# Performance work log

Measured on AMD Instinct MI355X. Metric: run time of the kernel, lower is better.

## Reference

```python
import jax, jax.numpy as jnp
import numpy as np

TOL_CONTACT = 0.01  # contact tolerance from signed_dis


def _knn_pair(ref_pts, ref_nrm, q_pts, k):
    """Signed distance from each query point to the surface of one other object.

    ref_pts/ref_nrm: [Nr,3] reference object points (in plane frame) and normals.
    q_pts: [Nq,3] query object points (in plane frame). Returns [Nq].
    """
    # brute-force squared distances [Nq, Nr] (same math as tra.nearest_neighbor)
    sq = (jnp.sum(q_pts * q_pts, -1)[:, None]
          - 2.0 * (q_pts @ ref_pts.T)
          + jnp.sum(ref_pts * ref_pts, -1)[None, :])
    negd, idx = jax.lax.top_k(-sq, k)                  # k nearest per query: [Nq,k]
    dist = jnp.sqrt(jnp.maximum(-negd, 0.0))           # euclidean distances
    near = ref_pts[idx]                                # [Nq,k,3] gathered surface pts
    near_n = ref_nrm[idx]                              # [Nq,k,3] gathered normals
    grad = near - q_pts[:, None, :]
    grad = grad / jnp.linalg.norm(grad, axis=-1, keepdims=True)
    insides = jnp.sum(near_n * grad, axis=-1) > 0      # einsum('okij,okij->oki')
    inside = jnp.sum(insides, axis=-1) > k * 0.8       # majority vote over k
    # nearest-neighbor distance, sign-flipped when inside
    return jnp.where(inside, -dist[:, 0], dist[:, 0])


def reference(points, est_T, plane_T, k):
    M, N, _ = points.shape
    # transform object points into plane frame
    T = jnp.linalg.inv(plane_T)[None] @ est_T          # [M,4,4]
    xyz = points[..., :3]
    nrm = points[..., 3:6]
    pts_pl = jnp.einsum('mij,mnj->mni', T[:, :3, :3], xyz) + T[:, None, :3, 3]
    sd_plane = pts_pl[..., 2]                          # plane signed distance [M,N]

    # signed distance of object b's points to every other object o: pair[b,o,:]
    pair = jax.vmap(
        lambda q: jax.vmap(lambda rp, rn: _knn_pair(rp, rn, q, k))(pts_pl, nrm)
    )(pts_pl)                                          # [M,M,N]
    big = jnp.asarray(jnp.finfo(pair.dtype).max, pair.dtype)
    pair = jnp.where(jnp.eye(M, dtype=bool)[:, :, None], big, pair)
    sd_obj = jnp.min(pair, axis=1)                     # min over other objects [M,N]

    signed_distance = jnp.minimum(sd_plane, sd_obj)
    intersects = signed_distance < -TOL_CONTACT
    return signed_distance, intersects


def setup_inputs() -> dict:
    key = jax.random.key(0)
    kp, kn, kt, kpl = jax.random.split(key, 4)
    M, N = 4, 3072
    # objects offset from each other so pairwise nearest distances are > 0
    xyz = jax.random.normal(kp, (M, N, 3), jnp.float32) * 0.05 \
        + jnp.arange(M, dtype=jnp.float32)[:, None, None] * 0.3
    nrm = jax.random.normal(kn, (M, N, 3), jnp.float32)
    nrm = nrm / jnp.linalg.norm(nrm, axis=-1, keepdims=True)
    points = jnp.concatenate([xyz, nrm], axis=-1)      # [M,N,6]

    def rigid(k_, n):
        q, _ = jnp.linalg.qr(jax.random.normal(k_, (n, 3, 3), jnp.float32))
        t = jax.random.normal(jax.random.fold_in(k_, 7), (n, 3), jnp.float32) * 0.1
        T = jnp.zeros((n, 4, 4), jnp.float32)
        T = T.at[:, :3, :3].set(q).at[:, :3, 3].set(t).at[:, 3, 3].set(1.0)
        return T

    est_T = rigid(kt, M)        # per-object estimated transforms [M,4,4]
    plane_T = rigid(kpl, 1)[0]  # plane transform [4,4]
    return {"points": points, "est_T": est_T, "plane_T": plane_T, "k": 10}
```

## Files before the change

kernel.cpp:

```cpp
#include <hip/hip_runtime.h>
#include <math.h>

#define M_OBJ 4
#define N_PTS 3072
#define K_NN  10
#define NSLOT (M_OBJ - 1)
#define QPB   64
#define SEG   4
#define SEGN  (N_PTS / SEG)
#define MSTR  10

__device__ inline void make_T(const float* __restrict__ E,
                              const float* __restrict__ P,
                              float T[3][4]) {
    float Pi[3][4];
#pragma unroll
    for (int i = 0; i < 3; ++i) {
#pragma unroll
        for (int j = 0; j < 3; ++j) Pi[i][j] = P[j * 4 + i];
        Pi[i][3] = -(P[0 * 4 + i] * P[3] + P[1 * 4 + i] * P[7] + P[2 * 4 + i] * P[11]);
    }
#pragma unroll
    for (int i = 0; i < 3; ++i) {
#pragma unroll
        for (int j = 0; j < 4; ++j) {
            float acc = (j == 3) ? Pi[i][3] : 0.0f;
#pragma unroll
            for (int kk = 0; kk < 3; ++kk) acc += Pi[i][kk] * E[kk * 4 + j];
            T[i][j] = acc;
        }
    }
}

__device__ __forceinline__ void insert10(float s, int id, float bs[K_NN], int bi[K_NN]) {
    bs[0] = s; bi[0] = id;
#pragma unroll
    for (int t = 0; t < K_NN - 1; ++t) {
        if (bs[t] > bs[t + 1]) {
            float a = bs[t]; bs[t] = bs[t + 1]; bs[t + 1] = a;
            int   b = bi[t]; bi[t] = bi[t + 1]; bi[t + 1] = b;
        }
    }
}

__device__ __forceinline__ float score(const float4 p, float qx, float qy, float qz) {
    return fmaf(p.x, qx, fmaf(p.y, qy, fmaf(p.z, qz, -p.w)));
}

__global__ __launch_bounds__(256, 3) void pair_kernel(
        const float* __restrict__ points,
        const float* __restrict__ estT,
        const float* __restrict__ planeT,
        float* __restrict__ pair_sd) {
    __shared__ float4 sref[N_PTS];
    __shared__ unsigned short mbuf[128 * MSTR];

    const int pidx  = blockIdx.x;
    const int q     = pidx / NSLOT;
    const int rs    = pidx % NSLOT;
    const int r     = rs + (rs >= q ? 1 : 0);
    const int tid   = threadIdx.x;
    const int seg   = tid >> 6;
    const int qlane = tid & 63;

    float Tq[3][4], Tr[3][4];
    make_T(estT + q * 16, planeT, Tq);
    make_T(estT + r * 16, planeT, Tr);

    for (int j = tid; j < N_PTS; j += 256) {
        const float* p = points + (size_t)(r * N_PTS + j) * 6;
        float2 xy = *(const float2*)p;
        float  z  = p[2];
        float px = Tr[0][0] * xy.x + Tr[0][1] * xy.y + Tr[0][2] * z + Tr[0][3];
        float py = Tr[1][0] * xy.x + Tr[1][1] * xy.y + Tr[1][2] * z + Tr[1][3];
        float pz = Tr[2][0] * xy.x + Tr[2][1] * xy.y + Tr[2][2] * z + Tr[2][3];
        float w  = 0.5f * (px * px + py * py + pz * pz);
        sref[j] = make_float4(px, py, pz, w);
    }
    __syncthreads();

    const int nq = blockIdx.y * QPB + qlane;
    const float* qp = points + (size_t)(q * N_PTS + nq) * 6;
    float2 qxy = *(const float2*)qp;
    float  qzz = qp[2];
    const float qx = Tq[0][0] * qxy.x + Tq[0][1] * qxy.y + Tq[0][2] * qzz + Tq[0][3];
    const float qy = Tq[1][0] * qxy.x + Tq[1][1] * qxy.y + Tq[1][2] * qzz + Tq[1][3];
    const float qz = Tq[2][0] * qxy.x + Tq[2][1] * qxy.y + Tq[2][2] * qzz + Tq[2][3];
    const float qq = qx * qx + qy * qy + qz * qz;

    float bs[K_NN]; int bi[K_NN];
#pragma unroll
    for (int i = 0; i < K_NN; ++i) { bs[i] = -3.4e38f; bi[i] = 0; }

    const int j0 = seg * SEGN;

#pragma unroll
    for (int i = 0; i < K_NN; ++i)
        insert10(score(sref[j0 + i], qx, qy, qz), j0 + i, bs, bi);

    for (int c = 0; c < SEGN / 64; ++c) {
        const int jj = j0 + c * 64;
        const float bs0 = bs[0];
        unsigned w0 = 0u, w1 = 0u;
#pragma unroll
        for (int b = 0; b < 32; ++b)
            w0 |= (score(sref[jj + b], qx, qy, qz) > bs0) ? (1u << b) : 0u;
#pragma unroll
        for (int b = 0; b < 32; ++b)
            w1 |= (score(sref[jj + 32 + b], qx, qy, qz) > bs0) ? (1u << b) : 0u;
        if (c == 0) w0 &= ~1023u;

        if (__any((w0 | w1) != 0u)) {
            while (__any(w0 != 0u)) {
                if (w0) {
                    const int b = __builtin_ctz(w0); w0 &= w0 - 1u;
                    const int id = jj + b;
                    const float s = score(sref[id], qx, qy, qz);
                    if (s > bs[0]) insert10(s, id, bs, bi);
                }
            }
            while (__any(w1 != 0u)) {
                if (w1) {
                    const int b = __builtin_ctz(w1); w1 &= w1 - 1u;
                    const int id = jj + 32 + b;
                    const float s = score(sref[id], qx, qy, qz);
                    if (s > bs[0]) insert10(s, id, bs, bi);
                }
            }
        }
    }

    __syncthreads();
    if (seg >= 2) {
        const int slot = tid - 128;
#pragma unroll
        for (int i = 0; i < K_NN; ++i) mbuf[slot * MSTR + i] = (unsigned short)bi[i];
    }
    __syncthreads();
    if (seg < 2) {
        const int src = (seg * 64 + qlane) * MSTR;
#pragma unroll
        for (int i = 0; i < K_NN; ++i) {
            const int id = mbuf[src + i];
            const float s = score(sref[id], qx, qy, qz);
            if (s > bs[0]) insert10(s, id, bs, bi);
        }
    }
    __syncthreads();
    if (seg == 1) {
#pragma unroll
        for (int i = 0; i < K_NN; ++i) mbuf[qlane * MSTR + i] = (unsigned short)bi[i];
    }
    __syncthreads();
    if (seg == 0) {
        const int src = qlane * MSTR;
#pragma unroll
        for (int i = 0; i < K_NN; ++i) {
            const int id = mbuf[src + i];
            const float s = score(sref[id], qx, qy, qz);
            if (s > bs[0]) insert10(s, id, bs, bi);
        }

        int votes = 0;
#pragma unroll
        for (int i = 0; i < K_NN; ++i) {
            const int id = bi[i];
            float4 p = sref[id];
            float gx = p.x - qx, gy = p.y - qy, gz = p.z - qz;
            const float* np_ = points + (size_t)(r * N_PTS + id) * 6 + 3;
            votes += (np_[0] * gx + np_[1] * gy + np_[2] * gz > 0.0f) ? 1 : 0;
        }

        float sq = fmaxf(fmaf(-2.0f, bs[K_NN - 1], qq), 0.0f);
        float d0 = sqrtf(sq);
        float sd = (votes > 8) ? -d0 : d0;
        pair_sd[((size_t)q * NSLOT + rs) * N_PTS + nq] = sd;
    }
}

__global__ __launch_bounds__(256) void reduce_kernel(
        const float* __restrict__ points,
        const float* __restrict__ estT,
        const float* __restrict__ planeT,
        const float* __restrict__ pair_sd,
        float* __restrict__ out) {
    int i = blockIdx.x * blockDim.x + threadIdx.x;
    if (i >= M_OBJ * N_PTS) return;
    int m = i / N_PTS, n = i % N_PTS;

    float T[3][4];
    make_T(estT + m * 16, planeT, T);
    const float* p = points + (size_t)i * 6;
    float zpl = T[2][0] * p[0] + T[2][1] * p[1] + T[2][2] * p[2] + T[2][3];

    float sd = zpl;
#pragma unroll
    for (int rs = 0; rs < NSLOT; ++rs)
        sd = fminf(sd, pair_sd[((size_t)m * NSLOT + rs) * N_PTS + n]);

    out[i] = sd;
    out[M_OBJ * N_PTS + i] = (sd < -0.01f) ? 1.0f : 0.0f;
}

extern "C" void kernel_launch(void* const* d_in, const int* in_sizes, int n_in,
                              void* d_out, int out_size, void* d_ws, size_t ws_size,
                              hipStream_t stream) {
    const float* points = (const float*)d_in[0];
    const float* estT   = (const float*)d_in[1];
    const float* planeT = (const float*)d_in[2];

    float* pair_sd = (float*)d_ws;

    dim3 gridB(M_OBJ * NSLOT, N_PTS / QPB);
    pair_kernel<<<gridB, 256, 0, stream>>>(points, estT, planeT, pair_sd);

    int total = M_OBJ * N_PTS;
    reduce_kernel<<<(total + 255) / 256, 256, 0, stream>>>(points, estT, planeT,
                                                           pair_sd, (float*)d_out);
}
```

Baseline: 139.5 us.

## Pack inside-vote bit into score LSB and use med3 sorted insertion

Drops the index array from the per-thread top-k list. The normal-dot-product vote bit is computed when a candidate is inserted and packed into the score's low bit, and insertion uses a branchless fmed3 chain instead of compare-swap. The list is seeded from a strided warm-up sample of 1/16 of the segment so the gate starts tight, and both bitmask loops are merged into one. The cross-segment merge exchanges packed floats rather than indices. The cost is a global normal load for every inserted candidate, and packing the bit slightly perturbs score ordering.

```diff
diff --git a/kernel.cpp b/kernel.cpp
--- a/kernel.cpp
+++ b/kernel.cpp
@@ -8,7 +8,9 @@
 #define QPB   64
 #define SEG   4
 #define SEGN  (N_PTS / SEG)
-#define MSTR  10
+#define NCHUNK (SEGN / 64)
+#define WSTRIDE 16
+#define NWARM (SEGN / WSTRIDE)
 
 __device__ inline void make_T(const float* __restrict__ E,
                               const float* __restrict__ P,
@@ -32,19 +34,11 @@
     }
 }
 
-__device__ __forceinline__ void insert10(float s, int id, float bs[K_NN], int bi[K_NN]) {
-    bs[0] = s; bi[0] = id;
-#pragma unroll
-    for (int t = 0; t < K_NN - 1; ++t) {
-        if (bs[t] > bs[t + 1]) {
-            float a = bs[t]; bs[t] = bs[t + 1]; bs[t + 1] = a;
-            int   b = bi[t]; bi[t] = bi[t + 1]; bi[t + 1] = b;
-        }
-    }
-}
-
-__device__ __forceinline__ float score(const float4 p, float qx, float qy, float qz) {
-    return fmaf(p.x, qx, fmaf(p.y, qy, fmaf(p.z, qz, -p.w)));
+__device__ __forceinline__ void insertv(float v, float bs[K_NN]) {
+#pragma unroll
+    for (int i = 0; i < K_NN - 1; ++i)
+        bs[i] = __builtin_amdgcn_fmed3f(v, bs[i], bs[i + 1]);
+    bs[K_NN - 1] = fmaxf(v, bs[K_NN - 1]);
 }
 
 __global__ __launch_bounds__(256, 3) void pair_kernel(
@@ -53,7 +47,7 @@
         const float* __restrict__ planeT,
         float* __restrict__ pair_sd) {
     __shared__ float4 sref[N_PTS];
-    __shared__ unsigned short mbuf[128 * MSTR];
+    __shared__ float  mbuf[128 * K_NN];
 
     const int pidx  = blockIdx.x;
     const int q     = pidx / NSLOT;
@@ -88,44 +82,55 @@
     const float qz = Tq[2][0] * qxy.x + Tq[2][1] * qxy.y + Tq[2][2] * qzz + Tq[2][3];
     const float qq = qx * qx + qy * qy + qz * qz;
 
-    float bs[K_NN]; int bi[K_NN];
-#pragma unroll
-    for (int i = 0; i < K_NN; ++i) { bs[i] = -3.4e38f; bi[i] = 0; }
+    const float* nrm_base = points + (size_t)r * N_PTS * 6 + 3;
+
+    auto cand_packed = [&](int id) -> float {
+        float4 p = sref[id];
+        float s = fmaf(p.x, qx, fmaf(p.y, qy, fmaf(p.z, qz, -p.w)));
+        const float* nb = nrm_base + (size_t)id * 6;
+        float gx = p.x - qx, gy = p.y - qy, gz = p.z - qz;
+        float dv = fmaf(nb[0], gx, fmaf(nb[1], gy, nb[2] * gz));
+        unsigned su = (__float_as_uint(s) & ~1u) | (dv > 0.0f ? 1u : 0u);
+        return __uint_as_float(su);
+    };
+
+    float bs[K_NN];
+#pragma unroll
+    for (int i = 0; i < K_NN; ++i) bs[i] = -3.4e38f;
 
     const int j0 = seg * SEGN;
 
-#pragma unroll
-    for (int i = 0; i < K_NN; ++i)
-        insert10(score(sref[j0 + i], qx, qy, qz), j0 + i, bs, bi);
-
-    for (int c = 0; c < SEGN / 64; ++c) {
+#pragma unroll 4
+    for (int t = 0; t < NWARM; ++t)
+        insertv(cand_packed(j0 + t * WSTRIDE), bs);
+
+    for (int c = 0; c < NCHUNK; ++c) {
         const int jj = j0 + c * 64;
-        const float bs0 = bs[0];
+        const float gate = __uint_as_float(__float_as_uint(bs[0]) & ~1u);
         unsigned w0 = 0u, w1 = 0u;
 #pragma unroll
-        for (int b = 0; b < 32; ++b)
-            w0 |= (score(sref[jj + b], qx, qy, qz) > bs0) ? (1u << b) : 0u;
-#pragma unroll
-        for (int b = 0; b < 32; ++b)
-            w1 |= (score(sref[jj + 32 + b], qx, qy, qz) > bs0) ? (1u << b) : 0u;
-        if (c == 0) w0 &= ~1023u;
-
-        if (__any((w0 | w1) != 0u)) {
-            while (__any(w0 != 0u)) {
-                if (w0) {
-                    const int b = __builtin_ctz(w0); w0 &= w0 - 1u;
-                    const int id = jj + b;
-                    const float s = score(sref[id], qx, qy, qz);
-                    if (s > bs[0]) insert10(s, id, bs, bi);
-                }
+        for (int b = 0; b < 32; ++b) {
+            float4 p = sref[jj + b];
+            float s = fmaf(p.x, qx, fmaf(p.y, qy, fmaf(p.z, qz, -p.w)));
+            w0 |= (s > gate) ? (1u << b) : 0u;
+        }
+#pragma unroll
+        for (int b = 0; b < 32; ++b) {
+            float4 p = sref[jj + 32 + b];
+            float s = fmaf(p.x, qx, fmaf(p.y, qy, fmaf(p.z, qz, -p.w)));
+            w1 |= (s > gate) ? (1u << b) : 0u;
+        }
+        w0 &= ~0x00010001u;
+        w1 &= ~0x00010001u;
+
+        while (__any((w0 | w1) != 0u)) {
+            if (w0) {
+                const int b = __builtin_ctz(w0); w0 &= w0 - 1u;
+                insertv(cand_packed(jj + b), bs);
             }
-            while (__any(w1 != 0u)) {
-                if (w1) {
-                    const int b = __builtin_ctz(w1); w1 &= w1 - 1u;
-                    const int id = jj + 32 + b;
-                    const float s = score(sref[id], qx, qy, qz);
-                    if (s > bs[0]) insert10(s, id, bs, bi);
-                }
+            if (w1) {
+                const int b = __builtin_ctz(w1); w1 &= w1 - 1u;
+                insertv(cand_packed(jj + 32 + b), bs);
             }
         }
     }
@@ -134,44 +139,31 @@
     if (seg >= 2) {
         const int slot = tid - 128;
 #pragma unroll
-        for (int i = 0; i < K_NN; ++i) mbuf[slot * MSTR + i] = (unsigned short)bi[i];
+        for (int i = 0; i < K_NN; ++i) mbuf[slot * K_NN + i] = bs[i];
     }
     __syncthreads();
     if (seg < 2) {
-        const int src = (seg * 64 + qlane) * MSTR;
-#pragma unroll
-        for (int i = 0; i < K_NN; ++i) {
-            const int id = mbuf[src + i];
-            const float s = score(sref[id], qx, qy, qz);
-            if (s > bs[0]) insert10(s, id, bs, bi);
-        }
+        const int src = (seg * 64 + qlane) * K_NN;
+#pragma unroll
+        for (int i = 0; i < K_NN; ++i) insertv(mbuf[src + i], bs);
     }
     __syncthreads();
     if (seg == 1) {
 #pragma unroll
-        for (int i = 0; i < K_NN; ++i) mbuf[qlane * MSTR + i] = (unsigned short)bi[i];
+        for (int i = 0; i < K_NN; ++i) mbuf[qlane * K_NN + i] = bs[i];
     }
     __syncthreads();
     if (seg == 0) {
-        const int src = qlane * MSTR;
-#pragma unroll
-        for (int i = 0; i < K_NN; ++i) {
-            const int id = mbuf[src + i];
-            const float s = score(sref[id], qx, qy, qz);
-            if (s > bs[0]) insert10(s, id, bs, bi);
-        }
+        const int src = qlane * K_NN;
+#pragma unroll
+        for (int i = 0; i < K_NN; ++i) insertv(mbuf[src + i], bs);
 
         int votes = 0;
 #pragma unroll
-        for (int i = 0; i < K_NN; ++i) {
-            const int id = bi[i];
-            float4 p = sref[id];
-            float gx = p.x - qx, gy = p.y - qy, gz = p.z - qz;
-            const float* np_ = points + (size_t)(r * N_PTS + id) * 6 + 3;
-            votes += (np_[0] * gx + np_[1] * gy + np_[2] * gz > 0.0f) ? 1 : 0;
-        }
-
-        float sq = fmaxf(fmaf(-2.0f, bs[K_NN - 1], qq), 0.0f);
+        for (int i = 0; i < K_NN; ++i) votes += (__float_as_uint(bs[i]) & 1u);
+
+        const float s1 = __uint_as_float(__float_as_uint(bs[K_NN - 1]) & ~1u);
+        float sq = fmaxf(fmaf(-2.0f, s1, qq), 0.0f);
         float d0 = sqrtf(sq);
         float sd = (votes > 8) ? -d0 : d0;
         pair_sd[((size_t)q * NSLOT + rs) * N_PTS + nq] = sd;
```

Measured after the change: 128.2 us. -8.1%, faster.
